# Kernel tuning notes

Measured on AMD Instinct MI355X. Metric: run time of the kernel, lower is better.

The kernel has to match this reference:

```python
import jax, jax.numpy as jnp
import numpy as np

EPS = 1e-7  # keras.backend.epsilon()


def setup_inputs() -> dict:
    key = jax.random.key(0)
    kx, kw, ku = jax.random.split(key, 3)
    B, S, F = 16, 4096, 512
    x = jax.random.normal(kx, (B, S, F), dtype=jnp.float32)
    # glorot-uniform-scaled weights
    limW = np.sqrt(6.0 / (F + F)).astype(np.float32)
    W = jax.random.uniform(kw, (F, F), dtype=jnp.float32, minval=-limW, maxval=limW)
    b = jnp.zeros((F,), dtype=jnp.float32)
    limu = np.sqrt(6.0 / (F + 1)).astype(np.float32)
    u = jax.random.uniform(ku, (F,), dtype=jnp.float32, minval=-limu, maxval=limu)
    return {"x": x, "W": W, "b": b, "u": u}


def reference(x, W, b, u):
    # x: [B,S,F]  W: [F,F]  b: [F]  u: [F]
    h = jnp.tanh(jnp.einsum('bsf,fg->bsg', x, W) + b)   # [B,S,F]
    scores = jnp.einsum('bsf,f->bs', h, u)              # [B,S]
    e = jnp.exp(scores)
    # NOTE: faithful to the source, normalization is GLOBAL over all B*S scores
    a = e / (jnp.sum(e) + EPS)                          # [B,S]
    out = jnp.einsum('bsf,bs->bf', x, a)                # [B,F] weighted-sum pool over steps
    return out
```

## Files before the change

kernel.cpp:

```cpp
#include <hip/hip_runtime.h>
#include <stdint.h>

#define EPSV 1e-7f
#define FDIM 512
#define BK 64
#define NROWS 65536

typedef __bf16 bf16_t;
typedef bf16_t bf16x8 __attribute__((ext_vector_type(8)));
typedef unsigned short ushort8 __attribute__((ext_vector_type(8)));
typedef float f32x4 __attribute__((ext_vector_type(4)));

#define AS1 __attribute__((address_space(1)))
#define AS3 __attribute__((address_space(3)))

__device__ __forceinline__ unsigned short f2bf(float f) {
  union { float f; unsigned int u; } c; c.f = f;
  unsigned int u = c.u;
  unsigned int r = u + 0x7fffu + ((u >> 16) & 1u);
  return (unsigned short)(r >> 16);
}
__device__ __forceinline__ float bf2f(unsigned short s) {
  union { unsigned int u; float f; } c; c.u = ((unsigned int)s) << 16;
  return c.f;
}

__device__ __forceinline__ float fast_tanh(float x) {
  x = fminf(15.0f, fmaxf(-15.0f, x));
  float t = __expf(2.0f * x);
  return 1.0f - 2.0f * __builtin_amdgcn_rcpf(t + 1.0f);
}

__global__ void convert_W(const float* __restrict__ W, unsigned short* __restrict__ Wt) {
  __shared__ unsigned short tile[32][34];
  const int t = threadIdx.x;
  const int tx = t & 31, ty = t >> 5;
  const int bn = blockIdx.x & 15, bk = blockIdx.x >> 4;
  const int k0 = bk * 32, n0 = bn * 32;
#pragma unroll
  for (int i = 0; i < 4; ++i) {
    int r = ty + i * 8;
    tile[r][tx] = f2bf(W[(size_t)(k0 + r) * FDIM + n0 + tx]);
  }
  __syncthreads();
#pragma unroll
  for (int i = 0; i < 4; ++i) {
    int r = ty + i * 8;
    Wt[(size_t)(n0 + r) * FDIM + k0 + tx] = tile[tx][r];
  }
}

__global__ __launch_bounds__(256) void convert_x(const float* __restrict__ x,
                                                 unsigned short* __restrict__ xbf) {
  size_t i = ((size_t)blockIdx.x * 256 + threadIdx.x) * 8;
  float4 lo = *(const float4*)(x + i);
  float4 hi = *(const float4*)(x + i + 4);
  ushort8 v;
  v[0] = f2bf(lo.x); v[1] = f2bf(lo.y); v[2] = f2bf(lo.z); v[3] = f2bf(lo.w);
  v[4] = f2bf(hi.x); v[5] = f2bf(hi.y); v[6] = f2bf(hi.z); v[7] = f2bf(hi.w);
  *(ushort8*)(xbf + i) = v;
}

template <bool ABF>
__global__ __launch_bounds__(256, 4) void gemm_score(
    const float* __restrict__ x, const unsigned short* __restrict__ xbf,
    const unsigned short* __restrict__ Wt,
    const float* __restrict__ bvec, const float* __restrict__ uvec,
    float* __restrict__ spart) {
  __shared__ unsigned short sA[128 * BK];
  __shared__ unsigned short sB[128 * BK];
  __shared__ float score_s[128];
  __shared__ float ub_s[128], bb_s[128];

  const int t = threadIdx.x;
  const int lane = t & 63;
  const int w = t >> 6;
  const int wm = w & 1;
  const int wn = w >> 1;
  const int quad = lane >> 4;
  const int l15 = lane & 15;
  const int nch = blockIdx.x >> 9;
  const int rt = blockIdx.x & 511;
  const int m0 = rt * 128;
  const int col0 = nch * 128;

  if (t < 128) {
    score_s[t] = 0.0f;
    ub_s[t] = uvec[col0 + t];
    bb_s[t] = bvec[col0 + t];
  }

  f32x4 acc[4][4];
#pragma unroll
  for (int mi = 0; mi < 4; ++mi)
#pragma unroll
    for (int ni = 0; ni < 4; ++ni) acc[mi][ni] = (f32x4){0.f, 0.f, 0.f, 0.f};

  for (int kc = 0; kc < FDIM / BK; ++kc) {
    const int kbase = kc * BK;
    if constexpr (ABF) {
#pragma unroll
      for (int i = 0; i < 4; ++i) {
        int rb = w * 32 + i * 8;
        int rl = rb + (lane >> 3);
        int j = (lane & 7) ^ (rl & 7);
        const unsigned short* g =
            xbf + (size_t)(m0 + rl) * FDIM + kbase + j * 8;
        unsigned short* l = (unsigned short*)(sA + rb * 64);
        __builtin_amdgcn_global_load_lds((AS1 void*)(g), (AS3 void*)(l), 16, 0, 0);
      }
    } else {
#pragma unroll
      for (int p = 0; p < 4; ++p) {
        int slot = t + 256 * p;
        int row = slot >> 3;
        int j = (slot & 7) ^ (row & 7);
        const float* g = x + (size_t)(m0 + row) * FDIM + kbase + j * 8;
        float4 lo = *(const float4*)g;
        float4 hi = *(const float4*)(g + 4);
        ushort8 v;
        v[0] = f2bf(lo.x); v[1] = f2bf(lo.y); v[2] = f2bf(lo.z); v[3] = f2bf(lo.w);
        v[4] = f2bf(hi.x); v[5] = f2bf(hi.y); v[6] = f2bf(hi.z); v[7] = f2bf(hi.w);
        *(ushort8*)(void*)(sA + slot * 8) = v;
      }
    }
#pragma unroll
    for (int i = 0; i < 4; ++i) {
      int nb = w * 32 + i * 8;
      int nl = nb + (lane >> 3);
      int j = (lane & 7) ^ (nl & 7);
      const unsigned short* g =
          Wt + (size_t)(col0 + nl) * FDIM + kbase + j * 8;
      unsigned short* l = (unsigned short*)(sB + nb * 64);
      __builtin_amdgcn_global_load_lds((AS1 void*)(g), (AS3 void*)(l), 16, 0, 0);
    }
    __syncthreads();
#pragma unroll
    for (int ks = 0; ks < 2; ++ks) {
      bf16x8 af[4], bfr[4];
#pragma unroll
      for (int mi = 0; mi < 4; ++mi) {
        int row = wm * 64 + mi * 16 + l15;
        int phys = (ks * 4 + quad) ^ (row & 7);
        af[mi] = *(const bf16x8*)(const void*)(sA + row * 64 + phys * 8);
      }
#pragma unroll
      for (int ni = 0; ni < 4; ++ni) {
        int row = wn * 64 + ni * 16 + l15;
        int phys = (ks * 4 + quad) ^ (row & 7);
        bfr[ni] = *(const bf16x8*)(const void*)(sB + row * 64 + phys * 8);
      }
#pragma unroll
      for (int mi = 0; mi < 4; ++mi)
#pragma unroll
        for (int ni = 0; ni < 4; ++ni)
          acc[mi][ni] = __builtin_amdgcn_mfma_f32_16x16x32_bf16(
              af[mi], bfr[ni], acc[mi][ni], 0, 0, 0);
    }
    __syncthreads();
  }

  float sc[4][4];
#pragma unroll
  for (int mi = 0; mi < 4; ++mi)
#pragma unroll
    for (int r = 0; r < 4; ++r) sc[mi][r] = 0.0f;
#pragma unroll
  for (int ni = 0; ni < 4; ++ni) {
    int cl = wn * 64 + ni * 16 + l15;
    float uu = ub_s[cl], bb = bb_s[cl];
#pragma unroll
    for (int mi = 0; mi < 4; ++mi)
#pragma unroll
      for (int r = 0; r < 4; ++r)
        sc[mi][r] += uu * fast_tanh(acc[mi][ni][r] + bb);
  }
#pragma unroll
  for (int mi = 0; mi < 4; ++mi)
#pragma unroll
    for (int r = 0; r < 4; ++r) {
      float v = sc[mi][r];
      v += __shfl_xor(v, 1); v += __shfl_xor(v, 2);
      v += __shfl_xor(v, 4); v += __shfl_xor(v, 8);
      if (l15 == 0)
        atomicAdd(&score_s[wm * 64 + mi * 16 + quad * 4 + r], v);
    }
  __syncthreads();
  if (t < 128) spart[(size_t)nch * NROWS + m0 + t] = score_s[t];
}

__global__ void score_exp(float* __restrict__ spart, float* __restrict__ sumE) {
  __shared__ float ws_[4];
  const int t = threadIdx.x;
  const int i = blockIdx.x * 256 + t;
  float s = spart[i] + spart[i + NROWS] + spart[i + 2 * NROWS] + spart[i + 3 * NROWS];
  float e = __expf(s);
  spart[i] = e;
  float v = e;
  v += __shfl_xor(v, 1);  v += __shfl_xor(v, 2);  v += __shfl_xor(v, 4);
  v += __shfl_xor(v, 8);  v += __shfl_xor(v, 16); v += __shfl_xor(v, 32);
  if ((t & 63) == 0) ws_[t >> 6] = v;
  __syncthreads();
  if (t == 0) atomicAdd(sumE, ws_[0] + ws_[1] + ws_[2] + ws_[3]);
}

__global__ __launch_bounds__(256, 8) void pool_part(
    const unsigned short* __restrict__ xbf, const float* __restrict__ e,
    float* __restrict__ ppool) {
  __shared__ float e_s[32];
  __shared__ float red[4][FDIM];
  const int t = threadIdx.x;
  const int c8 = t & 63, rg = t >> 6;
  const int r0 = blockIdx.x * 32;
  if (t < 32) e_s[t] = e[r0 + t];
  __syncthreads();
  float a[8];
#pragma unroll
  for (int j = 0; j < 8; ++j) a[j] = 0.0f;
  for (int it = 0; it < 8; ++it) {
    int row = rg * 8 + it;
    ushort8 v = *(const ushort8*)(xbf + (size_t)(r0 + row) * FDIM + c8 * 8);
    float wg = e_s[row];
#pragma unroll
    for (int j = 0; j < 8; ++j) a[j] += bf2f(v[j]) * wg;
  }
  *(float4*)&red[rg][c8 * 8]     = (float4){a[0], a[1], a[2], a[3]};
  *(float4*)&red[rg][c8 * 8 + 4] = (float4){a[4], a[5], a[6], a[7]};
  __syncthreads();
  int c = t, c2 = t + 256;
  float s0 = red[0][c] + red[1][c] + red[2][c] + red[3][c];
  float s1 = red[0][c2] + red[1][c2] + red[2][c2] + red[3][c2];
  ppool[(size_t)blockIdx.x * FDIM + c]  = s0;
  ppool[(size_t)blockIdx.x * FDIM + c2] = s1;
}

__global__ __launch_bounds__(256) void pool_reduce(
    const float* __restrict__ ppool, const float* __restrict__ sumE,
    float* __restrict__ out) {
  const int i = blockIdx.x * 256 + threadIdx.x;
  const int b = i >> 9, f = i & 511;
  float s = 0.0f;
  const float* p = ppool + (size_t)b * 128 * FDIM + f;
  for (int c = 0; c < 128; ++c) s += p[(size_t)c * FDIM];
  out[i] = s / (*sumE + EPSV);
}

__global__ __launch_bounds__(256) void pool_k(
    const float* __restrict__ x, const float* __restrict__ e,
    const float* __restrict__ sumE, float* __restrict__ out) {
  __shared__ float e_s[128];
  __shared__ float4 red[128];
  const int t = threadIdx.x;
  const int b = blockIdx.x >> 5, chunk = blockIdx.x & 31;
  const int g0 = b * 4096 + chunk * 128;
  if (t < 128) e_s[t] = e[g0 + t];
  __syncthreads();
  const int parity = t >> 7, f4 = t & 127;
  float ax = 0.f, ay = 0.f, az = 0.f, aw = 0.f;
  for (int r = 0; r < 64; ++r) {
    int row = r * 2 + parity;
    const float4 xv = *(const float4*)(x + (size_t)(g0 + row) * FDIM + f4 * 4);
    float wgt = e_s[row];
    ax += xv.x * wgt; ay += xv.y * wgt; az += xv.z * wgt; aw += xv.w * wgt;
  }
  if (parity) red[f4] = (float4){ax, ay, az, aw};
  __syncthreads();
  if (!parity) {
    float4 o = red[f4];
    float inv = 1.0f / (*sumE + EPSV);
    float* op = out + (size_t)b * FDIM + f4 * 4;
    atomicAdd(op + 0, (ax + o.x) * inv);
    atomicAdd(op + 1, (ay + o.y) * inv);
    atomicAdd(op + 2, (az + o.z) * inv);
    atomicAdd(op + 3, (aw + o.w) * inv);
  }
}

extern "C" void kernel_launch(void* const* d_in, const int* in_sizes, int n_in,
                              void* d_out, int out_size, void* d_ws, size_t ws_size,
                              hipStream_t stream) {
  (void)in_sizes; (void)n_in;
  const float* x = (const float*)d_in[0];
  const float* W = (const float*)d_in[1];
  const float* b = (const float*)d_in[2];
  const float* u = (const float*)d_in[3];
  float* out = (float*)d_out;

  char* p = (char*)d_ws;
  unsigned short* Wt = (unsigned short*)p;            p += (size_t)FDIM * FDIM * 2;
  float* spart = (float*)p;                           p += (size_t)4 * NROWS * 4;
  float* sumE = (float*)p;                            p += 256;
  float* ppool = (float*)p;                           p += (size_t)2048 * FDIM * 4;
  unsigned short* xbf = (unsigned short*)p;           p += (size_t)NROWS * FDIM * 2;
  const size_t need = (size_t)(p - (char*)d_ws);
  const bool big = ws_size >= need;

  hipMemsetAsync(sumE, 0, sizeof(float), stream);
  convert_W<<<dim3(256), dim3(256), 0, stream>>>(W, Wt);

  if (big) {
    convert_x<<<dim3(NROWS * FDIM / (256 * 8)), dim3(256), 0, stream>>>(x, xbf);
    gemm_score<true><<<dim3(2048), dim3(256), 0, stream>>>(x, xbf, Wt, b, u, spart);
    score_exp<<<dim3(NROWS / 256), dim3(256), 0, stream>>>(spart, sumE);
    pool_part<<<dim3(2048), dim3(256), 0, stream>>>(xbf, spart, ppool);
    pool_reduce<<<dim3(32), dim3(256), 0, stream>>>(ppool, sumE, out);
  } else {
    hipMemsetAsync(d_out, 0, (size_t)out_size * sizeof(float), stream);
    gemm_score<false><<<dim3(2048), dim3(256), 0, stream>>>(x, xbf, Wt, b, u, spart);
    score_exp<<<dim3(NROWS / 256), dim3(256), 0, stream>>>(spart, sumE);
    pool_k<<<dim3(512), dim3(256), 0, stream>>>(x, spart, sumE, out);
  }
}
```

Measured before the change: 274.6 us.

## Fuse conversion kernels, fold score exp into pooling, load A fragments directly from global

The x and W bf16 conversions now run as a single launch, and the score-summing exp plus global-sum step is folded into the pooling kernel, removing two launches. The GEMM's A operand is no longer staged through shared memory: each lane reads its bf16x8 fragments straight from global memory. Dropping the LDS staging saves shared-memory traffic, but the direct loads are strided and uncoalesced, and the A tile is re-read by both column-half waves. The fallback path keeps the old f32 GEMM under new names.

```diff
diff --git a/kernel.cpp b/kernel.cpp
--- a/kernel.cpp
+++ b/kernel.cpp
@@ -31,43 +31,43 @@
   return 1.0f - 2.0f * __builtin_amdgcn_rcpf(t + 1.0f);
 }
 
-__global__ void convert_W(const float* __restrict__ W, unsigned short* __restrict__ Wt) {
+__global__ __launch_bounds__(256) void convert_fused(
+    const float* __restrict__ x, unsigned short* __restrict__ xbf,
+    const float* __restrict__ W, unsigned short* __restrict__ Wt) {
   __shared__ unsigned short tile[32][34];
   const int t = threadIdx.x;
-  const int tx = t & 31, ty = t >> 5;
-  const int bn = blockIdx.x & 15, bk = blockIdx.x >> 4;
-  const int k0 = bk * 32, n0 = bn * 32;
-#pragma unroll
-  for (int i = 0; i < 4; ++i) {
-    int r = ty + i * 8;
-    tile[r][tx] = f2bf(W[(size_t)(k0 + r) * FDIM + n0 + tx]);
-  }
-  __syncthreads();
-#pragma unroll
-  for (int i = 0; i < 4; ++i) {
-    int r = ty + i * 8;
-    Wt[(size_t)(n0 + r) * FDIM + k0 + tx] = tile[tx][r];
-  }
-}
-
-__global__ __launch_bounds__(256) void convert_x(const float* __restrict__ x,
-                                                 unsigned short* __restrict__ xbf) {
-  size_t i = ((size_t)blockIdx.x * 256 + threadIdx.x) * 8;
-  float4 lo = *(const float4*)(x + i);
-  float4 hi = *(const float4*)(x + i + 4);
-  ushort8 v;
-  v[0] = f2bf(lo.x); v[1] = f2bf(lo.y); v[2] = f2bf(lo.z); v[3] = f2bf(lo.w);
-  v[4] = f2bf(hi.x); v[5] = f2bf(hi.y); v[6] = f2bf(hi.z); v[7] = f2bf(hi.w);
-  *(ushort8*)(xbf + i) = v;
-}
-
-template <bool ABF>
-__global__ __launch_bounds__(256, 4) void gemm_score(
-    const float* __restrict__ x, const unsigned short* __restrict__ xbf,
+  if (blockIdx.x < 16384) {
+    size_t i = ((size_t)blockIdx.x * 256 + t) * 8;
+    float4 lo = *(const float4*)(x + i);
+    float4 hi = *(const float4*)(x + i + 4);
+    ushort8 v;
+    v[0] = f2bf(lo.x); v[1] = f2bf(lo.y); v[2] = f2bf(lo.z); v[3] = f2bf(lo.w);
+    v[4] = f2bf(hi.x); v[5] = f2bf(hi.y); v[6] = f2bf(hi.z); v[7] = f2bf(hi.w);
+    *(ushort8*)(xbf + i) = v;
+  } else {
+    const int bi = blockIdx.x - 16384;
+    const int tx = t & 31, ty = t >> 5;
+    const int bn = bi & 15, bk = bi >> 4;
+    const int k0 = bk * 32, n0 = bn * 32;
+#pragma unroll
+    for (int i = 0; i < 4; ++i) {
+      int r = ty + i * 8;
+      tile[r][tx] = f2bf(W[(size_t)(k0 + r) * FDIM + n0 + tx]);
+    }
+    __syncthreads();
+#pragma unroll
+    for (int i = 0; i < 4; ++i) {
+      int r = ty + i * 8;
+      Wt[(size_t)(n0 + r) * FDIM + k0 + tx] = tile[tx][r];
+    }
+  }
+}
+
+__global__ __launch_bounds__(256, 4) void gemm_score_bf(
+    const unsigned short* __restrict__ xbf,
     const unsigned short* __restrict__ Wt,
     const float* __restrict__ bvec, const float* __restrict__ uvec,
     float* __restrict__ spart) {
-  __shared__ unsigned short sA[128 * BK];
   __shared__ unsigned short sB[128 * BK];
   __shared__ float score_s[128];
   __shared__ float ub_s[128], bb_s[128];
@@ -96,34 +96,10 @@
 #pragma unroll
     for (int ni = 0; ni < 4; ++ni) acc[mi][ni] = (f32x4){0.f, 0.f, 0.f, 0.f};
 
+  const unsigned short* aptr = xbf + (size_t)(m0 + wm * 64 + l15) * FDIM + quad * 8;
+
   for (int kc = 0; kc < FDIM / BK; ++kc) {
     const int kbase = kc * BK;
-    if constexpr (ABF) {
-#pragma unroll
-      for (int i = 0; i < 4; ++i) {
-        int rb = w * 32 + i * 8;
-        int rl = rb + (lane >> 3);
-        int j = (lane & 7) ^ (rl & 7);
-        const unsigned short* g =
-            xbf + (size_t)(m0 + rl) * FDIM + kbase + j * 8;
-        unsigned short* l = (unsigned short*)(sA + rb * 64);
-        __builtin_amdgcn_global_load_lds((AS1 void*)(g), (AS3 void*)(l), 16, 0, 0);
-      }
-    } else {
-#pragma unroll
-      for (int p = 0; p < 4; ++p) {
-        int slot = t + 256 * p;
-        int row = slot >> 3;
-        int j = (slot & 7) ^ (row & 7);
-        const float* g = x + (size_t)(m0 + row) * FDIM + kbase + j * 8;
-        float4 lo = *(const float4*)g;
-        float4 hi = *(const float4*)(g + 4);
-        ushort8 v;
-        v[0] = f2bf(lo.x); v[1] = f2bf(lo.y); v[2] = f2bf(lo.z); v[3] = f2bf(lo.w);
-        v[4] = f2bf(hi.x); v[5] = f2bf(hi.y); v[6] = f2bf(hi.z); v[7] = f2bf(hi.w);
-        *(ushort8*)(void*)(sA + slot * 8) = v;
-      }
-    }
 #pragma unroll
     for (int i = 0; i < 4; ++i) {
       int nb = w * 32 + i * 8;
@@ -139,11 +115,9 @@
     for (int ks = 0; ks < 2; ++ks) {
       bf16x8 af[4], bfr[4];
 #pragma unroll
-      for (int mi = 0; mi < 4; ++mi) {
-        int row = wm * 64 + mi * 16 + l15;
-        int phys = (ks * 4 + quad) ^ (row & 7);
-        af[mi] = *(const bf16x8*)(const void*)(sA + row * 64 + phys * 8);
-      }
+      for (int mi = 0; mi < 4; ++mi)
+        af[mi] = *(const bf16x8*)(const void*)(
+            aptr + (size_t)(mi * 16) * FDIM + kbase + ks * 32);
 #pragma unroll
       for (int ni = 0; ni < 4; ++ni) {
         int row = wn * 64 + ni * 16 + l15;
@@ -189,30 +163,24 @@
   if (t < 128) spart[(size_t)nch * NROWS + m0 + t] = score_s[t];
 }
 
-__global__ void score_exp(float* __restrict__ spart, float* __restrict__ sumE) {
-  __shared__ float ws_[4];
-  const int t = threadIdx.x;
-  const int i = blockIdx.x * 256 + t;
-  float s = spart[i] + spart[i + NROWS] + spart[i + 2 * NROWS] + spart[i + 3 * NROWS];
-  float e = __expf(s);
-  spart[i] = e;
-  float v = e;
-  v += __shfl_xor(v, 1);  v += __shfl_xor(v, 2);  v += __shfl_xor(v, 4);
-  v += __shfl_xor(v, 8);  v += __shfl_xor(v, 16); v += __shfl_xor(v, 32);
-  if ((t & 63) == 0) ws_[t >> 6] = v;
-  __syncthreads();
-  if (t == 0) atomicAdd(sumE, ws_[0] + ws_[1] + ws_[2] + ws_[3]);
-}
-
-__global__ __launch_bounds__(256, 8) void pool_part(
-    const unsigned short* __restrict__ xbf, const float* __restrict__ e,
-    float* __restrict__ ppool) {
+__global__ __launch_bounds__(256, 8) void pool_score(
+    const unsigned short* __restrict__ xbf, const float* __restrict__ spart,
+    float* __restrict__ sumE, float* __restrict__ ppool) {
   __shared__ float e_s[32];
   __shared__ float red[4][FDIM];
   const int t = threadIdx.x;
   const int c8 = t & 63, rg = t >> 6;
   const int r0 = blockIdx.x * 32;
-  if (t < 32) e_s[t] = e[r0 + t];
+  if (t < 32) {
+    int i = r0 + t;
+    float s = spart[i] + spart[i + NROWS] + spart[i + 2 * NROWS] + spart[i + 3 * NROWS];
+    float e = __expf(s);
+    e_s[t] = e;
+    float v = e;
+    v += __shfl_xor(v, 1); v += __shfl_xor(v, 2); v += __shfl_xor(v, 4);
+    v += __shfl_xor(v, 8); v += __shfl_xor(v, 16);
+    if (t == 0) atomicAdd(sumE, v);
+  }
   __syncthreads();
   float a[8];
 #pragma unroll
@@ -245,6 +213,140 @@
   out[i] = s / (*sumE + EPSV);
 }
 
+__global__ void convert_W_f(const float* __restrict__ W, unsigned short* __restrict__ Wt) {
+  __shared__ unsigned short tile[32][34];
+  const int t = threadIdx.x;
+  const int tx = t & 31, ty = t >> 5;
+  const int bn = blockIdx.x & 15, bk = blockIdx.x >> 4;
+  const int k0 = bk * 32, n0 = bn * 32;
+#pragma unroll
+  for (int i = 0; i < 4; ++i) {
+    int r = ty + i * 8;
+    tile[r][tx] = f2bf(W[(size_t)(k0 + r) * FDIM + n0 + tx]);
+  }
+  __syncthreads();
+#pragma unroll
+  for (int i = 0; i < 4; ++i) {
+    int r = ty + i * 8;
+    Wt[(size_t)(n0 + r) * FDIM + k0 + tx] = tile[tx][r];
+  }
+}
+
+__global__ __launch_bounds__(256, 4) void gemm_score_f32(
+    const float* __restrict__ x, const unsigned short* __restrict__ Wt,
+    const float* __restrict__ bvec, const float* __restrict__ uvec,
+    float* __restrict__ spart) {
+  __shared__ unsigned short sA[128 * BK];
+  __shared__ unsigned short sB[128 * BK];
+  __shared__ float score_s[128];
+  __shared__ float ub_s[128], bb_s[128];
+  const int t = threadIdx.x;
+  const int lane = t & 63;
+  const int w = t >> 6;
+  const int wm = w & 1, wn = w >> 1;
+  const int quad = lane >> 4, l15 = lane & 15;
+  const int nch = blockIdx.x >> 9;
+  const int rt = blockIdx.x & 511;
+  const int m0 = rt * 128, col0 = nch * 128;
+  if (t < 128) { score_s[t] = 0.0f; ub_s[t] = uvec[col0 + t]; bb_s[t] = bvec[col0 + t]; }
+  f32x4 acc[4][4];
+#pragma unroll
+  for (int mi = 0; mi < 4; ++mi)
+#pragma unroll
+    for (int ni = 0; ni < 4; ++ni) acc[mi][ni] = (f32x4){0.f, 0.f, 0.f, 0.f};
+  for (int kc = 0; kc < FDIM / BK; ++kc) {
+    const int kbase = kc * BK;
+#pragma unroll
+    for (int p = 0; p < 4; ++p) {
+      int slot = t + 256 * p;
+      int row = slot >> 3;
+      int j = (slot & 7) ^ (row & 7);
+      const float* g = x + (size_t)(m0 + row) * FDIM + kbase + j * 8;
+      float4 lo = *(const float4*)g;
+      float4 hi = *(const float4*)(g + 4);
+      ushort8 v;
+      v[0] = f2bf(lo.x); v[1] = f2bf(lo.y); v[2] = f2bf(lo.z); v[3] = f2bf(lo.w);
+      v[4] = f2bf(hi.x); v[5] = f2bf(hi.y); v[6] = f2bf(hi.z); v[7] = f2bf(hi.w);
+      *(ushort8*)(void*)(sA + slot * 8) = v;
+    }
+#pragma unroll
+    for (int i = 0; i < 4; ++i) {
+      int nb = w * 32 + i * 8;
+      int nl = nb + (lane >> 3);
+      int j = (lane & 7) ^ (nl & 7);
+      const unsigned short* g = Wt + (size_t)(col0 + nl) * FDIM + kbase + j * 8;
+      unsigned short* l = (unsigned short*)(sB + nb * 64);
+      __builtin_amdgcn_global_load_lds((AS1 void*)(g), (AS3 void*)(l), 16, 0, 0);
+    }
+    __syncthreads();
+#pragma unroll
+    for (int ks = 0; ks < 2; ++ks) {
+      bf16x8 af[4], bfr[4];
+#pragma unroll
+      for (int mi = 0; mi < 4; ++mi) {
+        int row = wm * 64 + mi * 16 + l15;
+        int phys = (ks * 4 + quad) ^ (row & 7);
+        af[mi] = *(const bf16x8*)(const void*)(sA + row * 64 + phys * 8);
+      }
+#pragma unroll
+      for (int ni = 0; ni < 4; ++ni) {
+        int row = wn * 64 + ni * 16 + l15;
+        int phys = (ks * 4 + quad) ^ (row & 7);
+        bfr[ni] = *(const bf16x8*)(const void*)(sB + row * 64 + phys * 8);
+      }
+#pragma unroll
+      for (int mi = 0; mi < 4; ++mi)
+#pragma unroll
+        for (int ni = 0; ni < 4; ++ni)
+          acc[mi][ni] = __builtin_amdgcn_mfma_f32_16x16x32_bf16(
+              af[mi], bfr[ni], acc[mi][ni], 0, 0, 0);
+    }
+    __syncthreads();
+  }
+  float sc[4][4];
+#pragma unroll
+  for (int mi = 0; mi < 4; ++mi)
+#pragma unroll
+    for (int r = 0; r < 4; ++r) sc[mi][r] = 0.0f;
+#pragma unroll
+  for (int ni = 0; ni < 4; ++ni) {
+    int cl = wn * 64 + ni * 16 + l15;
+    float uu = ub_s[cl], bb = bb_s[cl];
+#pragma unroll
+    for (int mi = 0; mi < 4; ++mi)
+#pragma unroll
+      for (int r = 0; r < 4; ++r)
+        sc[mi][r] += uu * fast_tanh(acc[mi][ni][r] + bb);
+  }
+#pragma unroll
+  for (int mi = 0; mi < 4; ++mi)
+#pragma unroll
+    for (int r = 0; r < 4; ++r) {
+      float v = sc[mi][r];
+      v += __shfl_xor(v, 1); v += __shfl_xor(v, 2);
+      v += __shfl_xor(v, 4); v += __shfl_xor(v, 8);
+      if (l15 == 0)
+        atomicAdd(&score_s[wm * 64 + mi * 16 + quad * 4 + r], v);
+    }
+  __syncthreads();
+  if (t < 128) spart[(size_t)nch * NROWS + m0 + t] = score_s[t];
+}
+
+__global__ void score_exp(float* __restrict__ spart, float* __restrict__ sumE) {
+  __shared__ float ws_[4];
+  const int t = threadIdx.x;
+  const int i = blockIdx.x * 256 + t;
+  float s = spart[i] + spart[i + NROWS] + spart[i + 2 * NROWS] + spart[i + 3 * NROWS];
+  float e = __expf(s);
+  spart[i] = e;
+  float v = e;
+  v += __shfl_xor(v, 1);  v += __shfl_xor(v, 2);  v += __shfl_xor(v, 4);
+  v += __shfl_xor(v, 8);  v += __shfl_xor(v, 16); v += __shfl_xor(v, 32);
+  if ((t & 63) == 0) ws_[t >> 6] = v;
+  __syncthreads();
+  if (t == 0) atomicAdd(sumE, ws_[0] + ws_[1] + ws_[2] + ws_[3]);
+}
+
 __global__ __launch_bounds__(256) void pool_k(
     const float* __restrict__ x, const float* __restrict__ e,
     const float* __restrict__ sumE, float* __restrict__ out) {
@@ -296,17 +398,16 @@
   const bool big = ws_size >= need;
 
   hipMemsetAsync(sumE, 0, sizeof(float), stream);
-  convert_W<<<dim3(256), dim3(256), 0, stream>>>(W, Wt);
 
   if (big) {
-    convert_x<<<dim3(NROWS * FDIM / (256 * 8)), dim3(256), 0, stream>>>(x, xbf);
-    gemm_score<true><<<dim3(2048), dim3(256), 0, stream>>>(x, xbf, Wt, b, u, spart);
-    score_exp<<<dim3(NROWS / 256), dim3(256), 0, stream>>>(spart, sumE);
-    pool_part<<<dim3(2048), dim3(256), 0, stream>>>(xbf, spart, ppool);
+    convert_fused<<<dim3(16384 + 256), dim3(256), 0, stream>>>(x, xbf, W, Wt);
+    gemm_score_bf<<<dim3(2048), dim3(256), 0, stream>>>(xbf, Wt, b, u, spart);
+    pool_score<<<dim3(2048), dim3(256), 0, stream>>>(xbf, spart, sumE, ppool);
     pool_reduce<<<dim3(32), dim3(256), 0, stream>>>(ppool, sumE, out);
   } else {
     hipMemsetAsync(d_out, 0, (size_t)out_size * sizeof(float), stream);
-    gemm_score<false><<<dim3(2048), dim3(256), 0, stream>>>(x, xbf, Wt, b, u, spart);
+    convert_W_f<<<dim3(256), dim3(256), 0, stream>>>(W, Wt);
+    gemm_score_f32<<<dim3(2048), dim3(256), 0, stream>>>(x, Wt, b, u, spart);
     score_exp<<<dim3(NROWS / 256), dim3(256), 0, stream>>>(spart, sumE);
     pool_k<<<dim3(512), dim3(256), 0, stream>>>(x, spart, sumE, out);
   }
```

Result: slower. 314.9 us (+14.7%).
